# Performance work log

Measured on AMD Instinct MI355X. Metric: run time of the kernel, lower is better.

The kernel has to match this reference:

```python
import jax, jax.numpy as jnp
import numpy as np

N = 4096        # nodes (cells)
E = 131072      # edges (avg degree 32)
IN = 3000       # input features (genes)
HID = 128       # hidden dim per head
H = 4           # attention heads
LAT = 16        # latent dim
NEG_SLOPE = 0.2 # PyG GATConv leaky_relu slope


def _gat_sparse(x, src, dst, W, a_src, a_dst, b, concat):
    """PyG GATConv on an edge list (src -> dst, softmax grouped by dst)."""
    n = x.shape[0]
    h_, c = a_src.shape
    h = (x @ W).reshape(n, h_, c)                      # [N,H,C]
    e_src = (h * a_src[None]).sum(-1)                  # [N,H]
    e_dst = (h * a_dst[None]).sum(-1)                  # [N,H]
    e = jax.nn.leaky_relu(e_src[src] + e_dst[dst], NEG_SLOPE)  # [E,H]
    m = jax.ops.segment_max(e, dst, num_segments=n)
    ex = jnp.exp(e - m[dst])
    denom = jax.ops.segment_sum(ex, dst, num_segments=n)
    alpha = ex / (denom[dst] + 1e-16)                  # PyG softmax eps
    out = jax.ops.segment_sum(alpha[:, :, None] * h[src], dst, num_segments=n)
    out = out.reshape(n, h_ * c) if concat else out.mean(1)
    return out + b


def _gat_dense(x, W, a_src, a_dst, b, concat):
    """GATConv over the complete graph (the SVD low-rank reconstruction is
    generically fully dense, so to_sparse() keeps all N^2 entries; with
    used_edge_weight=False only the structure matters)."""
    n = x.shape[0]
    h_, c = a_src.shape
    h = (x @ W).reshape(n, h_, c)
    e_src = (h * a_src[None]).sum(-1)                  # [N,H]
    e_dst = (h * a_dst[None]).sum(-1)                  # [N,H]
    # scores[i (target), j (source), head]
    scores = jax.nn.leaky_relu(e_dst[:, None, :] + e_src[None, :, :], NEG_SLOPE)
    alpha = jax.nn.softmax(scores, axis=1)             # softmax over sources
    out = jnp.einsum('ijh,jhc->ihc', alpha, h)
    out = out.reshape(n, h_ * c) if concat else out.mean(1)
    return out + b


def setup_inputs() -> dict:
    key = jax.random.key(0)
    ks = jax.random.split(key, 16)
    s = 0.05
    x = jax.random.normal(ks[0], (N, IN), jnp.float32)
    src = jax.random.randint(ks[1], (E,), 0, N, jnp.int32)
    off = jax.random.randint(ks[2], (E,), 1, N, jnp.int32)
    dst = (src + off) % N                              # no self loops (PyG re-adds them)
    edge_index = jnp.stack([src, dst], axis=0)
    edge_attr = jax.random.uniform(ks[3], (E,), jnp.float32)
    D1 = H * HID
    return {
        'x': x, 'edge_index': edge_index, 'edge_attr': edge_attr,
        'W1': jax.random.normal(ks[4], (IN, D1), jnp.float32) * s,
        'a1_src': jax.random.normal(ks[5], (H, HID), jnp.float32) * s,
        'a1_dst': jax.random.normal(ks[6], (H, HID), jnp.float32) * s,
        'b1': jnp.zeros((D1,), jnp.float32),
        'Wm': jax.random.normal(ks[7], (D1, H * LAT), jnp.float32) * s,
        'am_src': jax.random.normal(ks[8], (H, LAT), jnp.float32) * s,
        'am_dst': jax.random.normal(ks[9], (H, LAT), jnp.float32) * s,
        'bm': jnp.zeros((LAT,), jnp.float32),
        'Ws': jax.random.normal(ks[10], (D1, H * LAT), jnp.float32) * s,
        'as_src': jax.random.normal(ks[11], (H, LAT), jnp.float32) * s,
        'as_dst': jax.random.normal(ks[12], (H, LAT), jnp.float32) * s,
        'bs': jnp.zeros((LAT,), jnp.float32),
    }


def reference(x, edge_index, edge_attr, W1, a1_src, a1_dst, b1,
              Wm, am_src, am_dst, bm, Ws, as_src, as_dst, bs):
    loops = jnp.arange(N, dtype=edge_index.dtype)
    src = jnp.concatenate([edge_index[0], loops])      # GATConv add_self_loops=True
    dst = jnp.concatenate([edge_index[1], loops])
    # branch 1: original sparse graph
    x1 = _gat_sparse(x, src, dst, W1, a1_src, a1_dst, b1, True)
    z_mean1 = _gat_sparse(x1, src, dst, Wm, am_src, am_dst, bm, False)
    z_log_std1 = _gat_sparse(x1, src, dst, Ws, as_src, as_dst, bs, False)
    # branch 2: SVD low-rank reconstructed adjacency => complete graph
    x2 = _gat_dense(x, W1, a1_src, a1_dst, b1, True)
    z_mean2 = _gat_dense(x2, Wm, am_src, am_dst, bm, False)
    z_log_std2 = _gat_dense(x2, Ws, as_src, as_dst, bs, False)
    return (z_mean1, z_log_std1, z_mean2, z_log_std2)
```

## Files before the change

kernel.cpp:

```cpp
#include <hip/hip_runtime.h>

typedef unsigned short u16;
typedef unsigned long long u64;
typedef __attribute__((ext_vector_type(8))) short short8;
typedef __attribute__((ext_vector_type(4))) float f32x4;

#define NN   4096
#define EE   131072
#define ETOT (EE + NN)
#define HH   4
#define IND  3000
#define KP   3008
#define D1   512
#define C1   128
#define C2   16

__device__ __forceinline__ float b2f(u16 u){
  union { unsigned int i; float f; } v; v.i = ((unsigned int)u) << 16; return v.f;
}
__device__ __forceinline__ u16 f2b(float f){
  unsigned int x = __float_as_uint(f);
  unsigned int r = (x + 0x7fffu + ((x >> 16) & 1u)) >> 16;
  return (u16)r;
}
__device__ __forceinline__ float lrelu(float x){ return x > 0.f ? x : 0.2f * x; }

__device__ __forceinline__ void glds16(const void* g, void* l){
  __builtin_amdgcn_global_load_lds(
      (const __attribute__((address_space(1))) unsigned int*)g,
      (__attribute__((address_space(3))) unsigned int*)l, 16, 0, 0);
}

__global__ void zero_out_kernel(float* p, int n){
  int i = blockIdx.x * blockDim.x + threadIdx.x;
  if (i < n) p[i] = 0.f;
}

__global__ __launch_bounds__(256) void cvtXW_kernel(const float* __restrict__ X,
    const float* __restrict__ W, u16* __restrict__ Xhi, u16* __restrict__ Xlo,
    u16* __restrict__ Whi, u16* __restrict__ Wlo){
  __shared__ float T[64][65];
  int b = blockIdx.x;
  if (b < 6016){
    int id = b * 256 + threadIdx.x;
    int m = id / 376, ch = id - m * 376;
    int k = ch * 8;
    float v[8];
    if (k + 8 <= IND){
      float4 a = *(const float4*)(X + (size_t)m * IND + k);
      float4 bb = *(const float4*)(X + (size_t)m * IND + k + 4);
      v[0]=a.x; v[1]=a.y; v[2]=a.z; v[3]=a.w; v[4]=bb.x; v[5]=bb.y; v[6]=bb.z; v[7]=bb.w;
    } else {
      #pragma unroll
      for (int j = 0; j < 8; ++j){ int kk = k + j; v[j] = (kk < IND) ? X[(size_t)m*IND + kk] : 0.f; }
    }
    u16 h8[8], l8[8];
    #pragma unroll
    for (int j = 0; j < 8; ++j){ h8[j] = f2b(v[j]); l8[j] = f2b(v[j] - b2f(h8[j])); }
    *(uint4*)(Xhi + (size_t)m * KP + k) = *(uint4*)h8;
    *(uint4*)(Xlo + (size_t)m * KP + k) = *(uint4*)l8;
  } else {
    int wb = b - 6016;
    int kb = wb % 47, nb = wb / 47;
    int k0 = kb * 64, n0 = nb * 64;
    int t = threadIdx.x;
    #pragma unroll
    for (int rr = 0; rr < 4; ++rr){
      int kl = (t >> 4) + rr * 16;
      int nn = (t & 15) * 4;
      int k = k0 + kl;
      float4 v = make_float4(0.f, 0.f, 0.f, 0.f);
      if (k < IND) v = *(const float4*)(W + (size_t)k * D1 + n0 + nn);
      T[kl][nn] = v.x; T[kl][nn+1] = v.y; T[kl][nn+2] = v.z; T[kl][nn+3] = v.w;
    }
    __syncthreads();
    int nloc = t >> 2, kseg = (t & 3) * 16;
    int n = n0 + nloc;
    #pragma unroll
    for (int c2 = 0; c2 < 2; ++c2){
      int kloc = kseg + c2 * 8;
      u16 h8[8], l8[8];
      #pragma unroll
      for (int j = 0; j < 8; ++j){
        float f = T[kloc + j][nloc];
        h8[j] = f2b(f); l8[j] = f2b(f - b2f(h8[j]));
      }
      *(uint4*)(Whi + (size_t)n * KP + k0 + kloc) = *(uint4*)h8;
      *(uint4*)(Wlo + (size_t)n * KP + k0 + kloc) = *(uint4*)l8;
    }
  }
}

__global__ __launch_bounds__(256) void cvtW2_kernel(const float* __restrict__ WM,
    const float* __restrict__ WS, u16* __restrict__ Wh, u16* __restrict__ Wl){
  __shared__ float T[64][65];
  int half = blockIdx.y;
  int k0 = blockIdx.x * 64;
  const float* W = half ? WS : WM;
  int t = threadIdx.x;
  #pragma unroll
  for (int p = 0; p < 4; ++p){
    int r = p * 16 + (t >> 4), c4 = (t & 15) * 4;
    float4 v = *(const float4*)(W + (size_t)(k0 + r) * 64 + c4);
    T[r][c4] = v.x; T[r][c4+1] = v.y; T[r][c4+2] = v.z; T[r][c4+3] = v.w;
  }
  __syncthreads();
  #pragma unroll
  for (int p = 0; p < 4; ++p){
    int n = p * 16 + (t >> 4), k4 = (t & 15) * 4;
    u16 h4[4], l4[4];
    #pragma unroll
    for (int j = 0; j < 4; ++j){
      float f = T[k4 + j][n];
      h4[j] = f2b(f); l4[j] = f2b(f - b2f(h4[j]));
    }
    size_t o = (size_t)(half * 64 + n) * 512 + k0 + k4;
    *(ushort4*)(Wh + o) = *(ushort4*)h4;
    *(ushort4*)(Wl + o) = *(ushort4*)l4;
  }
}

__global__ __launch_bounds__(512) void gemm_mfma(const u16* __restrict__ Xhi,
    const u16* __restrict__ Xlo, const u16* __restrict__ Whi, const u16* __restrict__ Wlo,
    float* __restrict__ Hh){
  __shared__ char smem[32768];
  u16* sAh = (u16*)smem;
  u16* sAl = (u16*)(smem + 8192);
  u16* sBh = (u16*)(smem + 16384);
  u16* sBl = (u16*)(smem + 24576);
  int t = threadIdx.x, lane = t & 63;
  int wv = __builtin_amdgcn_readfirstlane(t >> 6);
  int ksw = wv >> 2;
  int wr = (wv >> 1) & 1, wc = wv & 1;
  int bm = blockIdx.x * 64, bn = blockIdx.y * 64;
  f32x4 acc[2][2] = {};
  int srow = t >> 3;
  int sc = (t & 7) ^ (srow & 7);
  const char* gAh = (const char*)(Xhi + (size_t)(bm + srow) * KP) + sc * 16;
  const char* gAl = (const char*)(Xlo + (size_t)(bm + srow) * KP) + sc * 16;
  const char* gBh = (const char*)(Whi + (size_t)(bn + srow) * KP) + sc * 16;
  const char* gBl = (const char*)(Wlo + (size_t)(bn + srow) * KP) + sc * 16;
  char* lAh = (char*)sAh + t * 16;
  char* lAl = (char*)sAl + t * 16;
  char* lBh = (char*)sBh + t * 16;
  char* lBl = (char*)sBl + t * 16;
  int r16 = lane & 15, kq = lane >> 4;
  int cc = ksw * 4 + kq;
  int aoff[2], boff[2];
  #pragma unroll
  for (int m = 0; m < 2; ++m){
    int arow = wr * 32 + m * 16 + r16;
    aoff[m] = arow * 128 + ((cc ^ (arow & 7)) * 16);
  }
  #pragma unroll
  for (int n = 0; n < 2; ++n){
    int brow = wc * 32 + n * 16 + r16;
    boff[n] = brow * 128 + ((cc ^ (brow & 7)) * 16);
  }
  for (int kb = 0; kb < KP * 2; kb += 128){
    glds16(gAh + kb, lAh);
    glds16(gAl + kb, lAl);
    glds16(gBh + kb, lBh);
    glds16(gBl + kb, lBl);
    __syncthreads();
    short8 ah[2], al[2], bh[2], bl[2];
    #pragma unroll
    for (int m = 0; m < 2; ++m){
      ah[m] = *(const short8*)((const char*)sAh + aoff[m]);
      al[m] = *(const short8*)((const char*)sAl + aoff[m]);
    }
    #pragma unroll
    for (int n = 0; n < 2; ++n){
      bh[n] = *(const short8*)((const char*)sBh + boff[n]);
      bl[n] = *(const short8*)((const char*)sBl + boff[n]);
    }
    #pragma unroll
    for (int m = 0; m < 2; ++m)
      #pragma unroll
      for (int n = 0; n < 2; ++n){
        acc[m][n] = __builtin_amdgcn_mfma_f32_16x16x32_bf16(ah[m], bh[n], acc[m][n], 0, 0, 0);
        acc[m][n] = __builtin_amdgcn_mfma_f32_16x16x32_bf16(ah[m], bl[n], acc[m][n], 0, 0, 0);
        acc[m][n] = __builtin_amdgcn_mfma_f32_16x16x32_bf16(al[m], bh[n], acc[m][n], 0, 0, 0);
      }
    __syncthreads();
  }
  float* red = (float*)smem;
  int pp = wr * 2 + wc;
  if (ksw){
    #pragma unroll
    for (int m = 0; m < 2; ++m)
      #pragma unroll
      for (int n = 0; n < 2; ++n)
        #pragma unroll
        for (int r = 0; r < 4; ++r)
          red[((((m*2+n)*4 + r) << 8) + (pp << 6)) + lane] = acc[m][n][r];
  }
  __syncthreads();
  if (!ksw){
    #pragma unroll
    for (int m = 0; m < 2; ++m)
      #pragma unroll
      for (int n = 0; n < 2; ++n){
        #pragma unroll
        for (int r = 0; r < 4; ++r)
          acc[m][n][r] += red[((((m*2+n)*4 + r) << 8) + (pp << 6)) + lane];
        int row = bm + wr * 32 + m * 16 + kq * 4;
        int col = bn + wc * 32 + n * 16 + r16;
        float* o = Hh + (size_t)row * D1 + col;
        #pragma unroll
        for (int r = 0; r < 4; ++r) o[(size_t)r * D1] = acc[m][n][r];
      }
  }
}

__global__ __launch_bounds__(256) void gemm_h_split(const float* __restrict__ X,
    const float* __restrict__ Wc, float* __restrict__ Hh){
  __shared__ u16 Ahs[64][40], Als[64][40], Bhs[64][40], Bls[64][40];
  int t = threadIdx.x, lane = t & 63, wave = t >> 6;
  int wr = wave >> 1, wcc = wave & 1;
  int bm = blockIdx.x * 64, bn = blockIdx.y * 64;
  f32x4 acc[2][2] = {};
  int arow = t >> 2, akc = (t & 3) << 3;
  int brow = t >> 3, bnc = (t & 7) << 3;
  for (int k0 = 0; k0 < IND; k0 += 32){
    float va[8];
    size_t abase = (size_t)(bm + arow) * IND + k0 + akc;
    if (k0 + akc + 8 <= IND){
      float4 r0 = *(const float4*)(X + abase);
      float4 r1 = *(const float4*)(X + abase + 4);
      va[0]=r0.x; va[1]=r0.y; va[2]=r0.z; va[3]=r0.w;
      va[4]=r1.x; va[5]=r1.y; va[6]=r1.z; va[7]=r1.w;
    } else {
      #pragma unroll
      for (int j = 0; j < 8; ++j){
        int k = k0 + akc + j;
        va[j] = (k < IND) ? X[abase + j] : 0.f;
      }
    }
    #pragma unroll
    for (int j = 0; j < 8; ++j){
      u16 hb = f2b(va[j]);
      Ahs[arow][akc + j] = hb;
      Als[arow][akc + j] = f2b(va[j] - b2f(hb));
    }
    {
      int gk = k0 + brow;
      float vb[8];
      if (gk < IND){
        const float* wp = Wc + (size_t)gk * D1 + bn + bnc;
        float4 r0 = *(const float4*)wp;
        float4 r1 = *(const float4*)(wp + 4);
        vb[0]=r0.x; vb[1]=r0.y; vb[2]=r0.z; vb[3]=r0.w;
        vb[4]=r1.x; vb[5]=r1.y; vb[6]=r1.z; vb[7]=r1.w;
      } else {
        #pragma unroll
        for (int j = 0; j < 8; ++j) vb[j] = 0.f;
      }
      #pragma unroll
      for (int j = 0; j < 8; ++j){
        u16 hb = f2b(vb[j]);
        Bhs[bnc + j][brow] = hb;
        Bls[bnc + j][brow] = f2b(vb[j] - b2f(hb));
      }
    }
    __syncthreads();
    int r16 = lane & 15, kq = (lane >> 4) << 3;
    short8 a0h = *(const short8*)&Ahs[wr*32      + r16][kq];
    short8 a1h = *(const short8*)&Ahs[wr*32 + 16 + r16][kq];
    short8 a0l = *(const short8*)&Als[wr*32      + r16][kq];
    short8 a1l = *(const short8*)&Als[wr*32 + 16 + r16][kq];
    short8 b0h = *(const short8*)&Bhs[wcc*32      + r16][kq];
    short8 b1h = *(const short8*)&Bhs[wcc*32 + 16 + r16][kq];
    short8 b0l = *(const short8*)&Bls[wcc*32      + r16][kq];
    short8 b1l = *(const short8*)&Bls[wcc*32 + 16 + r16][kq];
    acc[0][0] = __builtin_amdgcn_mfma_f32_16x16x32_bf16(a0h, b0h, acc[0][0], 0, 0, 0);
    acc[0][1] = __builtin_amdgcn_mfma_f32_16x16x32_bf16(a0h, b1h, acc[0][1], 0, 0, 0);
    acc[1][0] = __builtin_amdgcn_mfma_f32_16x16x32_bf16(a1h, b0h, acc[1][0], 0, 0, 0);
    acc[1][1] = __builtin_amdgcn_mfma_f32_16x16x32_bf16(a1h, b1h, acc[1][1], 0, 0, 0);
    acc[0][0] = __builtin_amdgcn_mfma_f32_16x16x32_bf16(a0h, b0l, acc[0][0], 0, 0, 0);
    acc[0][1] = __builtin_amdgcn_mfma_f32_16x16x32_bf16(a0h, b1l, acc[0][1], 0, 0, 0);
    acc[1][0] = __builtin_amdgcn_mfma_f32_16x16x32_bf16(a1h, b0l, acc[1][0], 0, 0, 0);
    acc[1][1] = __builtin_amdgcn_mfma_f32_16x16x32_bf16(a1h, b1l, acc[1][1], 0, 0, 0);
    acc[0][0] = __builtin_amdgcn_mfma_f32_16x16x32_bf16(a0l, b0h, acc[0][0], 0, 0, 0);
    acc[0][1] = __builtin_amdgcn_mfma_f32_16x16x32_bf16(a0l, b1h, acc[0][1], 0, 0, 0);
    acc[1][0] = __builtin_amdgcn_mfma_f32_16x16x32_bf16(a1l, b0h, acc[1][0], 0, 0, 0);
    acc[1][1] = __builtin_amdgcn_mfma_f32_16x16x32_bf16(a1l, b1h, acc[1][1], 0, 0, 0);
    __syncthreads();
  }
  int cr = (lane >> 4) << 2, cc = lane & 15;
  for (int i = 0; i < 2; ++i) for (int j = 0; j < 2; ++j){
    int row = bm + wr*32 + i*16 + cr;
    int col = bn + wcc*32 + j*16 + cc;
    float* o = Hh + (size_t)row * D1 + col;
    for (int r = 0; r < 4; ++r) o[(size_t)r * D1] = acc[i][j][r];
  }
}

__global__ __launch_bounds__(256) void transpose_h(const float* __restrict__ h,
    float* __restrict__ hT, u16* __restrict__ h16){
  __shared__ float T[64][65];
  int bm = blockIdx.x * 64, bc = blockIdx.y * 64;
  int t = threadIdx.x;
  #pragma unroll
  for (int p = 0; p < 4; ++p){
    int r = p * 16 + (t >> 4), c4 = (t & 15) * 4;
    float4 v = *(const float4*)(h + (size_t)(bm + r) * D1 + bc + c4);
    T[r][c4] = v.x; T[r][c4+1] = v.y; T[r][c4+2] = v.z; T[r][c4+3] = v.w;
    u16 q[4] = { f2b(v.x), f2b(v.y), f2b(v.z), f2b(v.w) };
    *(ushort4*)(h16 + (size_t)(bm + r) * D1 + bc + c4) = *(ushort4*)q;
  }
  __syncthreads();
  #pragma unroll
  for (int p = 0; p < 4; ++p){
    int c = p * 16 + (t >> 4), m4 = (t & 15) * 4;
    float4 o = make_float4(T[m4][c], T[m4+1][c], T[m4+2][c], T[m4+3][c]);
    *(float4*)(hT + (size_t)(bc + c) * NN + bm + m4) = o;
  }
}

__global__ __launch_bounds__(256) void evec128(const float* __restrict__ hsrc,
    const float* __restrict__ as_, const float* __restrict__ ad_,
    float* __restrict__ es, float* __restrict__ ed){
  int idx = blockIdx.x * 256 + threadIdx.x;
  if (idx >= NN * HH) return;
  int h = idx & 3;
  const float4* hp = (const float4*)(hsrc + (size_t)idx * C1);
  const float4* ap = (const float4*)(as_ + h * C1);
  const float4* dp = (const float4*)(ad_ + h * C1);
  float s1 = 0.f, s2 = 0.f;
  #pragma unroll
  for (int c = 0; c < 32; ++c){
    float4 v = hp[c], a = ap[c], d = dp[c];
    s1 += v.x*a.x + v.y*a.y + v.z*a.z + v.w*a.w;
    s2 += v.x*d.x + v.y*d.y + v.z*d.z + v.w*d.w;
  }
  es[idx] = s1; ed[idx] = s2;
}

__global__ void zero_kernel(int* p, int n){
  int i = blockIdx.x * blockDim.x + threadIdx.x;
  if (i < n) p[i] = 0;
}
__global__ void hist_kernel(const int* __restrict__ dstA, int* __restrict__ deg){
  int e = blockIdx.x * blockDim.x + threadIdx.x;
  if (e < ETOT){
    int d = (e < EE) ? dstA[e] : (e - EE);
    atomicAdd(&deg[d & (NN-1)], 1);
  }
}
__global__ __launch_bounds__(1024) void scan_kernel(const int* __restrict__ deg,
    int* __restrict__ off, int* __restrict__ cur){
  __shared__ int wsum[16];
  int t = threadIdx.x, lane = t & 63, wv = t >> 6;
  int v0 = deg[t*4], v1 = deg[t*4+1], v2 = deg[t*4+2], v3 = deg[t*4+3];
  int s = v0 + v1 + v2 + v3;
  int sc = s;
  #pragma unroll
  for (int o = 1; o < 64; o <<= 1){
    int y = __shfl_up(sc, o);
    if (lane >= o) sc += y;
  }
  if (lane == 63) wsum[wv] = sc;
  __syncthreads();
  int base = 0;
  #pragma unroll
  for (int i = 0; i < 16; ++i) base += (i < wv) ? wsum[i] : 0;
  int excl = base + sc - s;
  int a0 = excl, a1 = a0 + v0, a2 = a1 + v1, a3 = a2 + v2;
  off[t*4] = a0; off[t*4+1] = a1; off[t*4+2] = a2; off[t*4+3] = a3;
  cur[t*4] = a0; cur[t*4+1] = a1; cur[t*4+2] = a2; cur[t*4+3] = a3;
  if (t == 1023) off[4096] = base + sc;
}
__global__ void scatter_kernel(const int* __restrict__ srcA, const int* __restrict__ dstA,
    int* __restrict__ cur, int* __restrict__ sidx){
  int e = blockIdx.x * blockDim.x + threadIdx.x;
  if (e < ETOT){
    int s, d;
    if (e < EE){ s = srcA[e]; d = dstA[e]; } else { s = d = e - EE; }
    int pos = atomicAdd(&cur[d & (NN-1)], 1);
    pos = min(max(pos, 0), ETOT - 1);
    sidx[pos] = s & (NN-1);
  }
}

__global__ __launch_bounds__(256) void sparse1(const u16* __restrict__ h16,
    const float* __restrict__ es, const float* __restrict__ ed,
    const int* __restrict__ off, const int* __restrict__ sidx,
    const float* __restrict__ bias, u16* __restrict__ x1h, u16* __restrict__ x1l){
  int n = blockIdx.x, t = threadIdx.x, w = t >> 6;
  int o0 = off[n], deg = off[n+1] - o0;
  deg = min(max(deg, 0), ETOT);
  float edn = ed[n * HH + w];
  float dsum = 1e-16f, a0 = 0.f, a1 = 0.f;
  for (int e = 0; e < deg; ++e){
    int s = sidx[o0 + e] & (NN-1);
    float we = __expf(lrelu(es[s*HH + w] + edn));
    unsigned pk = *(const unsigned*)(h16 + ((size_t)s << 9) + 2*t);
    a0 = fmaf(we, b2f((u16)(pk & 0xffff)), a0);
    a1 = fmaf(we, b2f((u16)(pk >> 16)), a1);
    dsum += we;
  }
  float inv = 1.0f / dsum;
  float v0 = a0 * inv + bias[2*t];
  float v1 = a1 * inv + bias[2*t + 1];
  u16 h0 = f2b(v0), h1 = f2b(v1);
  u16 l0 = f2b(v0 - b2f(h0)), l1 = f2b(v1 - b2f(h1));
  size_t o = ((size_t)n << 9) + 2*t;
  *(unsigned*)(x1h + o) = (unsigned)h0 | ((unsigned)h1 << 16);
  *(unsigned*)(x1l + o) = (unsigned)l0 | ((unsigned)l1 << 16);
}

struct Sp2 { const float* h[2]; const float* es[2]; const float* ed[2];
             const float* bias[2]; float* out[2]; };
__global__ __launch_bounds__(64) void sparse2(Sp2 a,
    const int* __restrict__ off, const int* __restrict__ sidx){
  int n = blockIdx.x, sel = blockIdx.y;
  int lane = threadIdx.x, hh = lane >> 4;
  const float* hsrc = a.h[sel];
  const float* es = a.es[sel];
  const float* ed = a.ed[sel];
  int o0 = off[n], deg = off[n+1] - o0;
  deg = min(max(deg, 0), ETOT);
  float edn = ed[n * HH + hh];
  float dsum = 1e-16f, acc = 0.f;
  for (int e = 0; e < deg; ++e){
    int s = sidx[o0 + e] & (NN-1);
    float we = __expf(lrelu(es[s*HH + hh] + edn));
    acc = fmaf(we, hsrc[(size_t)s * 64 + lane], acc);
    dsum += we;
  }
  float v = acc / dsum;
  v += __shfl_xor(v, 16);
  v += __shfl_xor(v, 32);
  if (lane < 16) a.out[sel][(size_t)n * C2 + lane] = v * 0.25f + a.bias[sel][lane];
}

struct GsA {
  const u16* x1h; const u16* x1l; const u16* x2h; const u16* x2l;
  const u16* Wh; const u16* Wl;
  float* hm1; float* hs1; float* hm2T; float* hs2T;
  const float* AMS; const float* AMD; const float* ASS; const float* ASD;
  float* em1s; float* em1d; float* es1s; float* es1d;
  float* em2s; float* em2d; float* es2s; float* es2d;
};
__global__ __launch_bounds__(256) void gemm_small_fused(GsA a){
  __shared__ u16 sAh[32*64], sAl[32*64], sBh[128*64], sBl[128*64];
  int t = threadIdx.x, lane = t & 63;
  int wv = __builtin_amdgcn_readfirstlane(t >> 6);
  int src = blockIdx.y;
  int bm = blockIdx.x * 32;
  const u16* xh = src ? a.x2h : a.x1h;
  const u16* xl = src ? a.x2l : a.x1l;
  f32x4 acc[2][2] = {};
  int sarow = t >> 3, sac = (t & 7) ^ (sarow & 7);
  const char* gAh = (const char*)(xh + (size_t)(bm + sarow) * 512) + sac * 16;
  const char* gAl = (const char*)(xl + (size_t)(bm + sarow) * 512) + sac * 16;
  char* lAh = (char*)sAh + t * 16;
  char* lAl = (char*)sAl + t * 16;
  const char* gBh[4]; const char* gBl[4];
  #pragma unroll
  for (int q = 0; q < 4; ++q){
    int id = q * 256 + t;
    int br = id >> 3, bc = (id & 7) ^ (br & 7);
    gBh[q] = (const char*)(a.Wh + (size_t)br * 512) + bc * 16;
    gBl[q] = (const char*)(a.Wl + (size_t)br * 512) + bc * 16;
  }
  int r16 = lane & 15, kq = lane >> 4;
  int aoff[2][2], boff[2][2];
  #pragma unroll
  for (int m = 0; m < 2; ++m)
    #pragma unroll
    for (int ks = 0; ks < 2; ++ks){
      int arow = m * 16 + r16;
      int cc = ks * 4 + kq;
      aoff[m][ks] = arow * 128 + ((cc ^ (arow & 7)) * 16);
    }
  #pragma unroll
  for (int n = 0; n < 2; ++n)
    #pragma unroll
    for (int ks = 0; ks < 2; ++ks){
      int brow = wv * 32 + n * 16 + r16;
      int cc = ks * 4 + kq;
      boff[n][ks] = brow * 128 + ((cc ^ (brow & 7)) * 16);
    }
  for (int kb = 0; kb < 1024; kb += 128){
    glds16(gAh + kb, lAh);
    glds16(gAl + kb, lAl);
    #pragma unroll
    for (int q = 0; q < 4; ++q){
      glds16(gBh[q] + kb, (char*)sBh + (q * 256 + t) * 16);
      glds16(gBl[q] + kb, (char*)sBl + (q * 256 + t) * 16);
    }
    __syncthreads();
    #pragma unroll
    for (int ks = 0; ks < 2; ++ks){
      short8 ah[2], al[2], bh[2], bl[2];
      #pragma unroll
      for (int m = 0; m < 2; ++m){
        ah[m] = *(const short8*)((const char*)sAh + aoff[m][ks]);
        al[m] = *(const short8*)((const char*)sAl + aoff[m][ks]);
      }
      #pragma unroll
      for (int n = 0; n < 2; ++n){
        bh[n] = *(const short8*)((const char*)sBh + boff[n][ks]);
        bl[n] = *(const short8*)((const char*)sBl + boff[n][ks]);
      }
      #pragma unroll
      for (int m = 0; m < 2; ++m)
        #pragma unroll
        for (int n = 0; n < 2; ++n){
          acc[m][n] = __builtin_amdgcn_mfma_f32_16x16x32_bf16(ah[m], bh[n], acc[m][n], 0, 0, 0);
          acc[m][n] = __builtin_amdgcn_mfma_f32_16x16x32_bf16(ah[m], bl[n], acc[m][n], 0, 0, 0);
          acc[m][n] = __builtin_amdgcn_mfma_f32_16x16x32_bf16(al[m], bh[n], acc[m][n], 0, 0, 0);
        }
    }
    __syncthreads();
  }
  #pragma unroll
  for (int m = 0; m < 2; ++m){
    #pragma unroll
    for (int n = 0; n < 2; ++n){
      int colB = wv * 32 + n * 16;
      int half = colB >> 6;
      int colh = (colB & 63) + r16;
      int hh = (colB & 63) >> 4;
      int row0 = bm + m * 16 + kq * 4;
      if (src == 0){
        float* o = (half ? a.hs1 : a.hm1) + (size_t)row0 * 64 + colh;
        #pragma unroll
        for (int r = 0; r < 4; ++r) o[(size_t)r * 64] = acc[m][n][r];
      } else {
        float* oT = (half ? a.hs2T : a.hm2T) + (size_t)colh * NN + row0;
        *(float4*)oT = make_float4(acc[m][n][0], acc[m][n][1], acc[m][n][2], acc[m][n][3]);
      }
      const float* AS = half ? a.ASS : a.AMS;
      const float* AD = half ? a.ASD : a.AMD;
      float av = AS[colh], dv = AD[colh];
      float* esP = src ? (half ? a.es2s : a.em2s) : (half ? a.es1s : a.em1s);
      float* edP = src ? (half ? a.es2d : a.em2d) : (half ? a.es1d : a.em1d);
      #pragma unroll
      for (int r = 0; r < 4; ++r){
        float vs = acc[m][n][r] * av;
        float vd = acc[m][n][r] * dv;
        #pragma unroll
        for (int msk = 1; msk < 16; msk <<= 1){
          vs += __shfl_xor(vs, msk);
          vd += __shfl_xor(vd, msk);
        }
        if (r16 == 0){
          int rw = row0 + r;
          esP[rw * HH + hh] = vs;
          edP[rw * HH + hh] = vd;
        }
      }
    }
  }
}

struct RkA { const float* in[2]; float* us[2]; int* pm[2]; };
__global__ __launch_bounds__(1024) void rank_kernel(RkA a){
  int sid = blockIdx.y;
  int sel = sid >> 2, h = sid & 3;
  const float* evals = a.in[sel];
  __shared__ u64 K[NN];
  __shared__ int red[1024];
  int t = threadIdx.x;
  for (int i = t; i < NN; i += 1024){
    unsigned x = __float_as_uint(evals[i*HH + h]);
    x = (x & 0x80000000u) ? ~x : (x | 0x80000000u);
    K[i] = ((u64)x << 32) | (unsigned)i;
  }
  __syncthreads();
  int jl = t & 63, sp = t >> 6;
  int j = blockIdx.x * 64 + jl;
  u64 myk = K[j];
  int cnt = 0;
  int k0 = sp * 256;
  #pragma unroll 8
  for (int i = 0; i < 256; ++i)
    cnt += (K[k0 + i] < myk) ? 1 : 0;
  red[t] = cnt;
  __syncthreads();
  if (sp == 0){
    int rank = 0;
    #pragma unroll
    for (int s = 0; s < 16; ++s) rank += red[jl + 64*s];
    a.us[sel][h*NN + rank] = evals[j*HH + h];
    a.pm[sel][h*NN + rank] = j;
  }
}

struct PfxA { const float* T[2]; const int* pm[2]; const float* us[2];
              float* P1[2]; float* P2[2]; };
__global__ __launch_bounds__(512) void prefix_kernel(PfxA a, int C){
  int sel = blockIdx.y;
  int Cp = C + 1;
  int h = blockIdx.x / Cp, c = blockIdx.x % Cp;
  const float* Tsrc = a.T[sel];
  const int*   pm   = a.pm[sel] + h * NN;
  const float* us   = a.us[sel] + h * NN;
  float* P1 = a.P1[sel];
  float* P2 = a.P2[sel];
  const float* row = Tsrc + (size_t)(h * C + c) * NN;
  __shared__ float L1[NN], L2[NN];
  __shared__ float T1[8], T2[8], O1[9], O2[9];
  int t = threadIdx.x, lane = t & 63, w = t >> 6;
  size_t base = (size_t)h * (NN + 1);
  float run1 = 0.f, run2 = 0.f;
  for (int cc = 0; cc < 8; ++cc){
    int k = w * 512 + cc * 64 + lane;
    float u = us[k];
    float v = 1.0f;
    if (c < C){ int j = pm[k] & (NN-1); v = row[j]; }
    float t1 = __expf(u) * v;
    float t2 = __expf(0.2f * u) * v;
    float s1 = t1, s2 = t2;
    for (int o = 1; o < 64; o <<= 1){
      float y1 = __shfl_up(s1, o), y2 = __shfl_up(s2, o);
      if (lane >= o){ s1 += y1; s2 += y2; }
    }
    L1[k] = run1 + s1 - t1;
    L2[k] = run2 + s2 - t2;
    run1 += __shfl(s1, 63);
    run2 += __shfl(s2, 63);
  }
  if (lane == 63){ T1[w] = run1; T2[w] = run2; }
  __syncthreads();
  if (t == 0){
    float a1 = 0.f, a2 = 0.f;
    #pragma unroll
    for (int s = 0; s < 8; ++s){ O1[s] = a1; O2[s] = a2; a1 += T1[s]; a2 += T2[s]; }
    O1[8] = a1; O2[8] = a2;
  }
  __syncthreads();
  for (int i = t; i < NN; i += 512){
    P1[(base + i) * Cp + c] = L1[i] + O1[i >> 9];
    P2[(base + i) * Cp + c] = L2[i] + O2[i >> 9];
  }
  if (t == 0){
    P1[(base + NN) * Cp + c] = O1[8];
    P2[(base + NN) * Cp + c] = O2[8];
  }
}

template<int C, bool MEAN>
__device__ __forceinline__ void dense_body(const float* __restrict__ P1,
    const float* __restrict__ P2, const float* __restrict__ usort,
    const float* __restrict__ ed, const float* __restrict__ bias,
    float* __restrict__ outF, u16* __restrict__ outH, u16* __restrict__ outL, int i){
  constexpr int Cp = C + 1;
  constexpr int NC = HH * C;
  int t = threadIdx.x;
  __shared__ float Ed[HH], E2d[HH], Den[HH];
  __shared__ int   Kh[HH];
  __shared__ float vals[NC > 256 ? 1 : NC];
  if (t < HH){
    float d = ed[i*HH + t];
    float target = -d;
    const float* us = usort + t * NN;
    int lo = 0, hi = NN;
    while (lo < hi){ int mid = (lo + hi) >> 1; if (us[mid] < target) lo = mid + 1; else hi = mid; }
    Kh[t] = lo;
    float e1 = __expf(d), e2 = __expf(0.2f * d);
    Ed[t] = e1; E2d[t] = e2;
    size_t base = (size_t)t * (NN + 1);
    float p1N = P1[(base + NN) * Cp + C];
    float p1k = P1[(base + lo) * Cp + C];
    float p2k = P2[(base + lo) * Cp + C];
    Den[t] = e1 * (p1N - p1k) + e2 * p2k;
  }
  __syncthreads();
  if (!MEAN){
    for (int ch = t; ch < NC; ch += 256){
      int h = ch / C, c = ch % C;
      size_t base = (size_t)h * (NN + 1);
      float p1N = P1[(base + NN)    * Cp + c];
      float p1k = P1[(base + Kh[h]) * Cp + c];
      float p2k = P2[(base + Kh[h]) * Cp + c];
      float num = Ed[h] * (p1N - p1k) + E2d[h] * p2k;
      float val = num / Den[h] + bias[ch];
      u16 hb = f2b(val);
      outH[(size_t)i * NC + ch] = hb;
      outL[(size_t)i * NC + ch] = f2b(val - b2f(hb));
    }
  } else {
    if (t < NC){
      int h = t / C, c = t % C;
      size_t base = (size_t)h * (NN + 1);
      float p1N = P1[(base + NN)    * Cp + c];
      float p1k = P1[(base + Kh[h]) * Cp + c];
      float p2k = P2[(base + Kh[h]) * Cp + c];
      vals[t] = (Ed[h] * (p1N - p1k) + E2d[h] * p2k) / Den[h];
    }
    __syncthreads();
    if (t < C){
      float z = (vals[t] + vals[C + t] + vals[2*C + t] + vals[3*C + t]) * 0.25f + bias[t];
      outF[(size_t)i * C + t] = z;
    }
  }
}

__global__ __launch_bounds__(256) void dense_out1(const float* __restrict__ P1,
    const float* __restrict__ P2, const float* __restrict__ usort,
    const float* __restrict__ ed, const float* __restrict__ bias,
    u16* __restrict__ outH, u16* __restrict__ outL){
  dense_body<C1, false>(P1, P2, usort, ed, bias, nullptr, outH, outL, blockIdx.x);
}

struct Dn2 { const float* P1[2]; const float* P2[2]; const float* us[2];
             const float* ed[2]; const float* bias[2]; float* out[2]; };
__global__ __launch_bounds__(256) void dense_out2(Dn2 a){
  int s = blockIdx.y;
  dense_body<C2, true>(a.P1[s], a.P2[s], a.us[s], a.ed[s], a.bias[s], a.out[s],
                       nullptr, nullptr, blockIdx.x);
}

extern "C" void kernel_launch(void* const* d_in, const int* in_sizes, int n_in,
                              void* d_out, int out_size, void* d_ws, size_t ws_size,
                              hipStream_t stream){
  const float* X   = (const float*)d_in[0];
  const int*   EI  = (const int*)d_in[1];
  const float* W1  = (const float*)d_in[3];
  const float* A1S = (const float*)d_in[4];
  const float* A1D = (const float*)d_in[5];
  const float* B1  = (const float*)d_in[6];
  const float* WM  = (const float*)d_in[7];
  const float* AMS = (const float*)d_in[8];
  const float* AMD = (const float*)d_in[9];
  const float* BM  = (const float*)d_in[10];
  const float* WS  = (const float*)d_in[11];
  const float* ASS = (const float*)d_in[12];
  const float* ASD = (const float*)d_in[13];
  const float* BS  = (const float*)d_in[14];
  float* OUT = (float*)d_out;
  (void)in_sizes; (void)n_in;

  if (ws_size < (size_t)56 * 1024 * 1024){
    zero_out_kernel<<<dim3((out_size + 255)/256), 256, 0, stream>>>(OUT, out_size);
    return;
  }
  bool fast = (ws_size >= (size_t)68 * 1024 * 1024);

  const size_t MB = 1024 * 1024;
  char* w = (char*)d_ws;
  size_t o = 0;
  auto alloc = [&](size_t bytes) -> void* {
    void* p = w + o;
    o += (bytes + 255) & ~(size_t)255;
    return p;
  };
  int*   deg  = (int*)  alloc(NN * 4);
  int*   coff = (int*)  alloc((NN + 1) * 4);
  int*   cur  = (int*)  alloc(NN * 4);
  int*   sidx = (int*)  alloc((size_t)ETOT * 4);
  float* e1s  = (float*)alloc(NN * HH * 4);
  float* e1d  = (float*)alloc(NN * HH * 4);
  float* us1  = (float*)alloc(HH * NN * 4);
  int*   pm1  = (int*)  alloc(HH * NN * 4);
  float* em1s = (float*)alloc(NN * HH * 4);
  float* em1d = (float*)alloc(NN * HH * 4);
  float* es1s = (float*)alloc(NN * HH * 4);
  float* es1d = (float*)alloc(NN * HH * 4);
  float* em2s = (float*)alloc(NN * HH * 4);
  float* em2d = (float*)alloc(NN * HH * 4);
  float* es2s = (float*)alloc(NN * HH * 4);
  float* es2d = (float*)alloc(NN * HH * 4);
  float* us2m = (float*)alloc(HH * NN * 4);
  int*   pm2m = (int*)  alloc(HH * NN * 4);
  float* us2s = (float*)alloc(HH * NN * 4);
  int*   pm2s = (int*)  alloc(HH * NN * 4);
  u16*   Wh2  = (u16*)  alloc(128 * 512 * 2);
  u16*   Wl2  = (u16*)  alloc(128 * 512 * 2);
  float* h    = (float*)alloc((size_t)NN * D1 * 4);
  char*  BIG  = w + o;
  size_t szX = (size_t)NN * KP * 2, szW = (size_t)D1 * KP * 2;
  u16* Xhi = (u16*)BIG;
  u16* Xlo = (u16*)(BIG + szX);
  u16* Whi = (u16*)(BIG + 2*szX);
  u16* Wlo = (u16*)(BIG + 2*szX + szW);
  u16*   x1h = (u16*)  (BIG + 0*MB);
  u16*   x1l = (u16*)  (BIG + 4*MB);
  u16*   x2h = (u16*)  (BIG + 8*MB);
  u16*   x2l = (u16*)  (BIG + 12*MB);
  float* hT  = (float*)(BIG + 16*MB);
  u16*   h16 = (u16*)  (BIG + 24*MB);
  float* P1a = (float*)(BIG + 28*MB);
  float* P2a = (float*)(BIG + 37*MB);
  float* hm1  = (float*)(BIG + 16*MB);
  float* hs1  = (float*)(BIG + 17*MB);
  float* hm2T = (float*)(BIG + 18*MB);
  float* hs2T = (float*)(BIG + 19*MB);
  float* P1m  = (float*)(BIG + 20*MB);
  float* P2m  = (float*)(BIG + 21*MB + 512*1024);
  float* P1s  = (float*)(BIG + 23*MB);
  float* P2s  = (float*)(BIG + 24*MB + 512*1024);

  const int* srcA = EI;
  const int* dstA = EI + EE;

  cvtW2_kernel<<<dim3(8, 2), 256, 0, stream>>>(WM, WS, Wh2, Wl2);
  if (fast){
    cvtXW_kernel<<<dim3(6016 + 47*8), 256, 0, stream>>>(X, W1, Xhi, Xlo, Whi, Wlo);
    gemm_mfma<<<dim3(NN/64, D1/64), 512, 0, stream>>>(Xhi, Xlo, Whi, Wlo, h);
  } else {
    gemm_h_split<<<dim3(NN/64, D1/64), 256, 0, stream>>>(X, W1, h);
  }
  transpose_h<<<dim3(NN/64, D1/64), 256, 0, stream>>>(h, hT, h16);
  evec128<<<dim3(NN*HH/256), 256, 0, stream>>>(h, A1S, A1D, e1s, e1d);
  zero_kernel<<<dim3(16), 256, 0, stream>>>(deg, NN);
  hist_kernel<<<dim3((ETOT + 255)/256), 256, 0, stream>>>(dstA, deg);
  scan_kernel<<<dim3(1), 1024, 0, stream>>>(deg, coff, cur);
  scatter_kernel<<<dim3((ETOT + 255)/256), 256, 0, stream>>>(srcA, dstA, cur, sidx);
  sparse1<<<dim3(NN), 256, 0, stream>>>(h16, e1s, e1d, coff, sidx, B1, x1h, x1l);
  {
    RkA ra; ra.in[0] = e1s; ra.in[1] = e1s; ra.us[0] = us1; ra.us[1] = us1;
    ra.pm[0] = pm1; ra.pm[1] = pm1;
    rank_kernel<<<dim3(64, 4), 1024, 0, stream>>>(ra);
    PfxA pa; pa.T[0] = hT; pa.T[1] = hT; pa.pm[0] = pm1; pa.pm[1] = pm1;
    pa.us[0] = us1; pa.us[1] = us1; pa.P1[0] = P1a; pa.P1[1] = P1a;
    pa.P2[0] = P2a; pa.P2[1] = P2a;
    prefix_kernel<<<dim3(HH*(C1+1), 1), 512, 0, stream>>>(pa, C1);
    dense_out1<<<dim3(NN), 256, 0, stream>>>(P1a, P2a, us1, e1d, B1, x2h, x2l);
  }
  {
    GsA ga;
    ga.x1h = x1h; ga.x1l = x1l; ga.x2h = x2h; ga.x2l = x2l;
    ga.Wh = Wh2; ga.Wl = Wl2;
    ga.hm1 = hm1; ga.hs1 = hs1; ga.hm2T = hm2T; ga.hs2T = hs2T;
    ga.AMS = AMS; ga.AMD = AMD; ga.ASS = ASS; ga.ASD = ASD;
    ga.em1s = em1s; ga.em1d = em1d; ga.es1s = es1s; ga.es1d = es1d;
    ga.em2s = em2s; ga.em2d = em2d; ga.es2s = es2s; ga.es2d = es2d;
    gemm_small_fused<<<dim3(NN/32, 2), 256, 0, stream>>>(ga);
  }
  {
    Sp2 sp;
    sp.h[0] = hm1; sp.h[1] = hs1; sp.es[0] = em1s; sp.es[1] = es1s;
    sp.ed[0] = em1d; sp.ed[1] = es1d; sp.bias[0] = BM; sp.bias[1] = BS;
    sp.out[0] = OUT; sp.out[1] = OUT + (size_t)NN*C2;
    sparse2<<<dim3(NN, 2), 64, 0, stream>>>(sp, coff, sidx);
  }
  {
    RkA ra; ra.in[0] = em2s; ra.in[1] = es2s; ra.us[0] = us2m; ra.us[1] = us2s;
    ra.pm[0] = pm2m; ra.pm[1] = pm2s;
    rank_kernel<<<dim3(64, 8), 1024, 0, stream>>>(ra);
    PfxA pa; pa.T[0] = hm2T; pa.T[1] = hs2T; pa.pm[0] = pm2m; pa.pm[1] = pm2s;
    pa.us[0] = us2m; pa.us[1] = us2s; pa.P1[0] = P1m; pa.P1[1] = P1s;
    pa.P2[0] = P2m; pa.P2[1] = P2s;
    prefix_kernel<<<dim3(HH*(C2+1), 2), 512, 0, stream>>>(pa, C2);
    Dn2 dn;
    dn.P1[0] = P1m; dn.P1[1] = P1s; dn.P2[0] = P2m; dn.P2[1] = P2s;
    dn.us[0] = us2m; dn.us[1] = us2s; dn.ed[0] = em2d; dn.ed[1] = es2d;
    dn.bias[0] = BM; dn.bias[1] = BS;
    dn.out[0] = OUT + (size_t)2*NN*C2; dn.out[1] = OUT + (size_t)3*NN*C2;
    dense_out2<<<dim3(NN, 2), 256, 0, stream>>>(dn);
  }
}
```

Baseline: 387.5 us.

## Double-buffer LDS tiles in split-precision MFMA GEMM with async prefetch

```diff
diff --git a/kernel.cpp b/kernel.cpp
--- a/kernel.cpp
+++ b/kernel.cpp
@@ -123,11 +123,7 @@
 __global__ __launch_bounds__(512) void gemm_mfma(const u16* __restrict__ Xhi,
     const u16* __restrict__ Xlo, const u16* __restrict__ Whi, const u16* __restrict__ Wlo,
     float* __restrict__ Hh){
-  __shared__ char smem[32768];
-  u16* sAh = (u16*)smem;
-  u16* sAl = (u16*)(smem + 8192);
-  u16* sBh = (u16*)(smem + 16384);
-  u16* sBl = (u16*)(smem + 24576);
+  __shared__ u16 sbuf[2][4][4096];
   int t = threadIdx.x, lane = t & 63;
   int wv = __builtin_amdgcn_readfirstlane(t >> 6);
   int ksw = wv >> 2;
@@ -140,10 +136,6 @@
   const char* gAl = (const char*)(Xlo + (size_t)(bm + srow) * KP) + sc * 16;
   const char* gBh = (const char*)(Whi + (size_t)(bn + srow) * KP) + sc * 16;
   const char* gBl = (const char*)(Wlo + (size_t)(bn + srow) * KP) + sc * 16;
-  char* lAh = (char*)sAh + t * 16;
-  char* lAl = (char*)sAl + t * 16;
-  char* lBh = (char*)sBh + t * 16;
-  char* lBl = (char*)sBl + t * 16;
   int r16 = lane & 15, kq = lane >> 4;
   int cc = ksw * 4 + kq;
   int aoff[2], boff[2];
@@ -157,22 +149,37 @@
     int brow = wc * 32 + n * 16 + r16;
     boff[n] = brow * 128 + ((cc ^ (brow & 7)) * 16);
   }
-  for (int kb = 0; kb < KP * 2; kb += 128){
-    glds16(gAh + kb, lAh);
-    glds16(gAl + kb, lAl);
-    glds16(gBh + kb, lBh);
-    glds16(gBl + kb, lBl);
-    __syncthreads();
+
+  #define STAGE(step, b) do { int ko = (step) * 128;            \
+      glds16(gAh + ko, (char*)sbuf[b][0] + t * 16);             \
+      glds16(gAl + ko, (char*)sbuf[b][1] + t * 16);             \
+      glds16(gBh + ko, (char*)sbuf[b][2] + t * 16);             \
+      glds16(gBl + ko, (char*)sbuf[b][3] + t * 16);             \
+    } while (0)
+  #define BARRIER()  asm volatile("s_barrier" ::: "memory")
+  #define WAIT_V4()  asm volatile("s_waitcnt vmcnt(4)" ::: "memory")
+  #define WAIT_V0()  asm volatile("s_waitcnt vmcnt(0)" ::: "memory")
+
+  STAGE(0, 0);
+  STAGE(1, 1);
+  WAIT_V4();
+  BARRIER();
+  for (int i = 0; i < 47; ++i){
+    int cur = i & 1;
+    const char* pAh = (const char*)sbuf[cur][0];
+    const char* pAl = (const char*)sbuf[cur][1];
+    const char* pBh = (const char*)sbuf[cur][2];
+    const char* pBl = (const char*)sbuf[cur][3];
     short8 ah[2], al[2], bh[2], bl[2];
     #pragma unroll
     for (int m = 0; m < 2; ++m){
-      ah[m] = *(const short8*)((const char*)sAh + aoff[m]);
-      al[m] = *(const short8*)((const char*)sAl + aoff[m]);
+      ah[m] = *(const short8*)(pAh + aoff[m]);
+      al[m] = *(const short8*)(pAl + aoff[m]);
     }
     #pragma unroll
     for (int n = 0; n < 2; ++n){
-      bh[n] = *(const short8*)((const char*)sBh + boff[n]);
-      bl[n] = *(const short8*)((const char*)sBl + boff[n]);
+      bh[n] = *(const short8*)(pBh + boff[n]);
+      bl[n] = *(const short8*)(pBl + boff[n]);
     }
     #pragma unroll
     for (int m = 0; m < 2; ++m)
@@ -182,9 +189,20 @@
         acc[m][n] = __builtin_amdgcn_mfma_f32_16x16x32_bf16(ah[m], bl[n], acc[m][n], 0, 0, 0);
         acc[m][n] = __builtin_amdgcn_mfma_f32_16x16x32_bf16(al[m], bh[n], acc[m][n], 0, 0, 0);
       }
-    __syncthreads();
-  }
-  float* red = (float*)smem;
+    BARRIER();
+    if (i + 2 < 47){
+      STAGE(i + 2, cur);
+      WAIT_V4();
+    } else {
+      WAIT_V0();
+    }
+    BARRIER();
+  }
+  #undef STAGE
+  #undef BARRIER
+  #undef WAIT_V4
+  #undef WAIT_V0
+  float* red = (float*)sbuf;
   int pp = wr * 2 + wc;
   if (ksw){
     #pragma unroll
```

Result: no change. 380.6 us (-1.8%).
